# Optimization experiments

Measured on AMD Instinct MI355X. Metric: run time of the kernel, lower is better.

The kernel has to match this reference:

```python
import jax, jax.numpy as jnp
import numpy as np

Q, B, N, DIM, HEADS, CODES = 4, 8, 4096, 1024, 8, 1024
DH = DIM // HEADS  # codebook_dim = 128
SCALE = DH ** -0.5


def setup_inputs() -> dict:
    key = jax.random.key(0)
    k0, k1, k2, k3 = jax.random.split(key, 4)
    return {
        "x": jax.random.normal(k0, (B, N, DIM), jnp.float32),
        "codes": jax.random.normal(k1, (Q, HEADS, CODES, DH), jnp.float32),
        "wk": jax.random.normal(k2, (Q, HEADS, DH, DH), jnp.float32) * SCALE,
        "wv": jax.random.normal(k3, (Q, HEADS, DH, DH), jnp.float32) * SCALE,
    }


def _memcodes_layer(x, codes, wk, wv):
    """One Memcodes quantizer (eval path: hard argmax).
    x: [B,N,DIM]; codes: [H,C,DH]; wk/wv: [H,DH,DH].
    Returns quantized [B,N,DIM], indices [B,H,N]."""
    b, n, _ = x.shape
    q = x.reshape(b, n, HEADS, DH).transpose(0, 2, 1, 3) * SCALE  # [b,h,n,d]
    k = jnp.einsum('hnd,hdc->hnc', codes, wk)  # [h,C,d]
    v = jnp.einsum('hnd,hdc->hnc', codes, wv)  # [h,C,d]
    logits = jnp.einsum('bhid,hjd->bhij', q, k)  # [b,h,n,C]
    idx = jnp.argmax(logits, axis=-1)  # [b,h,n]
    # one_hot(idx) @ v == gather rows of v at idx
    out = jnp.take_along_axis(v[None], idx[..., None], axis=2)  # [b,h,n,d]
    out = out.transpose(0, 2, 1, 3).reshape(b, n, DIM)
    return out, idx


def reference(x, codes, wk, wv):
    residual = x
    quantized_out = jnp.zeros_like(x)
    all_indices = []
    for i in range(Q):  # fixed small loop over quantizer layers
        quantized, idx = _memcodes_layer(residual, codes[i], wk[i], wv[i])
        residual = residual - quantized
        quantized_out = quantized_out + quantized
        all_indices.append(idx)
    return quantized_out, jnp.stack(all_indices, axis=-1)  # [B,N,DIM], [B,H,N,Q]
```

## Files before the change

### kernel.cpp

```cpp
#include <hip/hip_runtime.h>
#include <math.h>

#define QL 4
#define BB 8
#define NN 4096
#define DIMF 1024
#define HH 8
#define CC 1024
#define DH 128

#define MARGIN 4e-3f

typedef __attribute__((ext_vector_type(4))) float f32x4;
typedef __attribute__((ext_vector_type(8))) short s16x8;

__device__ __forceinline__ unsigned short f2bf(float f) {
    unsigned int u = __float_as_uint(f);
    u = u + 0x7fffu + ((u >> 16) & 1u);
    return (unsigned short)(u >> 16);
}
__device__ __forceinline__ float bf2f(unsigned short b) {
    return __uint_as_float(((unsigned int)b) << 16);
}
__device__ __forceinline__ void dma16(const void* g, void* l) {
    __builtin_amdgcn_global_load_lds(
        (const __attribute__((address_space(1))) unsigned int*)g,
        (__attribute__((address_space(3))) unsigned int*)l, 16, 0, 0);
}

#define MFMA(a, bb, c) c = __builtin_amdgcn_mfma_f32_16x16x32_bf16(a, bb, c, 0, 0, 0)

__device__ __forceinline__ void upd(float& m1, float& m2, int& mi, float v, int c) {
    m2 = fmaxf(fminf(m1, v), m2);
    if (v > m1) { m1 = v; mi = c; }
}

__global__ __launch_bounds__(128) void kv_kernel(
    const float* __restrict__ codes, const float* __restrict__ wk,
    const float* __restrict__ wv, unsigned short* __restrict__ khi,
    unsigned short* __restrict__ klo, float* __restrict__ vbuf)
{
    __shared__ float sc[8][128];
    int bid = blockIdx.x;
    int cg  = bid & 127;
    int qh  = bid >> 7;
    int t   = threadIdx.x;

    const float* cbase = codes + ((size_t)qh * CC + (size_t)cg * 8) * DH;
    #pragma unroll
    for (int i = 0; i < 8; ++i) sc[i][t] = cbase[i * DH + t];
    __syncthreads();

    const float* wkb = wk + (size_t)qh * DH * DH;
    const float* wvb = wv + (size_t)qh * DH * DH;

    float ak[8], av[8];
    #pragma unroll
    for (int i = 0; i < 8; ++i) { ak[i] = 0.f; av[i] = 0.f; }

    for (int d = 0; d < DH; ++d) {
        float a = wkb[d * DH + t];
        float b = wvb[d * DH + t];
        #pragma unroll
        for (int i = 0; i < 8; ++i) {
            ak[i] = fmaf(sc[i][d], a, ak[i]);
            av[i] = fmaf(sc[i][d], b, av[i]);
        }
    }

    size_t base = ((size_t)qh * CC + (size_t)cg * 8) * DH + t;
    #pragma unroll
    for (int i = 0; i < 8; ++i) {
        float f = ak[i];
        unsigned short hb = f2bf(f);
        unsigned short lb = f2bf(f - bf2f(hb));
        khi[base + (size_t)i * DH]  = hb;
        klo[base + (size_t)i * DH]  = lb;
        vbuf[base + (size_t)i * DH] = av[i];
    }
}

__global__ __launch_bounds__(256, 2) void fused_kernel(
    const float* __restrict__ x, const unsigned short* __restrict__ khi,
    const unsigned short* __restrict__ klo, const float* __restrict__ vbuf,
    const float* __restrict__ codes, const float* __restrict__ wk,
    const float* __restrict__ wv, float* __restrict__ out)
{
    __shared__ __align__(16) char kstage[2][16384];
    __shared__ int    chosen[64];
    __shared__ float  smax1[64];
    __shared__ int    flagged[64];
    __shared__ int    hist[QL][64];
    __shared__ int    nflag;
    __shared__ float  rbuf32[DH];
    __shared__ double rbuf64[DH];
    __shared__ double pbuf[DH];
    __shared__ int    cand[64];
    __shared__ int    ncand;
    __shared__ int    bestc;
    __shared__ double bestv;

    const int t  = threadIdx.x;
    const int w  = t >> 6;
    const int l  = t & 63;
    const int lr = l & 15;
    const int lg = l >> 4;

    const int bid = blockIdx.x;
    const int h   = bid & 7;
    const int nt  = (bid >> 3) & 63;
    const int b   = bid >> 9;
    const int n0  = nt * 64;

    const int colE  = ((l & 15) << 4) ^ ((l >> 4) << 4) ^ (((l >> 3) & 1) << 5);
    const int loffE = ((l >> 4) << 8) + colE;
    const int loffO = loffE ^ 0x40;

    s16x8 rhi[4], rlo[4];
    {
        const int tok = w * 16 + lr;
        const float* xp = x + ((size_t)(b * NN + n0 + tok)) * DIMF + h * DH;
        #pragma unroll
        for (int ks = 0; ks < 4; ++ks) {
            const float* p = xp + ks * 32 + lg * 8;
            float4 a = *reinterpret_cast<const float4*>(p);
            float4 c = *reinterpret_cast<const float4*>(p + 4);
            float vv[8] = {a.x, a.y, a.z, a.w, c.x, c.y, c.z, c.w};
            s16x8 hi8, lo8;
            #pragma unroll
            for (int j = 0; j < 8; ++j) {
                unsigned short hb = f2bf(vv[j]);
                unsigned short lb = f2bf(vv[j] - bf2f(hb));
                hi8[j] = (short)hb; lo8[j] = (short)lb;
            }
            rhi[ks] = hi8; rlo[ks] = lo8;
        }
    }
    if (t == 0) nflag = 0;
    __syncthreads();

    for (int q = 0; q < QL; ++q) {
        const unsigned short* khq = khi + (size_t)(q * HH + h) * CC * DH;
        const unsigned short* klq = klo + (size_t)(q * HH + h) * CC * DH;
        const float* vq = vbuf + (size_t)(q * HH + h) * CC * DH;
        const char* khc = (const char*)khq;
        const char* klc = (const char*)klq;

        auto stage4 = [&](int buf, int chunk) {
            const char* gh = khc + chunk * 8192 + w * 2048;
            const char* gl = klc + chunk * 8192 + w * 2048;
            char* lb = &kstage[buf][0] + w * 2048;
            dma16(gh + loffE, lb);
            dma16(gh + 1024 + loffO, lb + 1024);
            dma16(gl + loffE, lb + 8192);
            dma16(gl + 1024 + loffO, lb + 8192 + 1024);
        };

        float bv[4], b2[4];
        int   bi[4];
        #pragma unroll
        for (int r = 0; r < 4; ++r) {
            bv[r] = -INFINITY; b2[r] = -INFINITY; bi[r] = 0;
        }

        stage4(0, 0);

        for (int ct = 0; ct < 32; ++ct) {
            const int cur = ct & 1;
            if (ct < 31) {
                stage4(cur ^ 1, ct + 1);
                asm volatile("s_waitcnt vmcnt(4)" ::: "memory");
            } else {
                asm volatile("s_waitcnt vmcnt(0)" ::: "memory");
            }
            __builtin_amdgcn_sched_barrier(0);
            __builtin_amdgcn_s_barrier();
            __builtin_amdgcn_sched_barrier(0);

            const char* Bb = &kstage[cur][0];
            f32x4 a00 = {0.f,0.f,0.f,0.f}, a01 = {0.f,0.f,0.f,0.f};

            #pragma unroll
            for (int ks = 0; ks < 4; ++ks) {
                const int swz = ((ks * 64 + lg * 16) ^ ((lr & 7) << 4)) ^ ((ks >> 1) << 5);
                const char* p0 = Bb + (lr)      * 256 + swz;
                const char* p1 = Bb + (16 + lr) * 256 + swz;
                s16x8 bh0 = *reinterpret_cast<const s16x8*>(p0);
                s16x8 bh1 = *reinterpret_cast<const s16x8*>(p1);
                s16x8 bl0 = *reinterpret_cast<const s16x8*>(p0 + 8192);
                s16x8 bl1 = *reinterpret_cast<const s16x8*>(p1 + 8192);

                __builtin_amdgcn_s_setprio(1);
                MFMA(rhi[ks], bh0, a00); MFMA(rhi[ks], bh1, a01);
                MFMA(rlo[ks], bh0, a00); MFMA(rlo[ks], bh1, a01);
                MFMA(rhi[ks], bl0, a00); MFMA(rhi[ks], bl1, a01);
                __builtin_amdgcn_s_setprio(0);
            }

            {
                const int cb = ct * 32 + lr;
                #pragma unroll
                for (int r = 0; r < 4; ++r) {
                    upd(bv[r], b2[r], bi[r], a00[r], cb);
                    upd(bv[r], b2[r], bi[r], a01[r], cb + 16);
                }
            }

            __builtin_amdgcn_sched_barrier(0);
            __builtin_amdgcn_s_barrier();
            __builtin_amdgcn_sched_barrier(0);
        }

        #pragma unroll
        for (int r = 0; r < 4; ++r) {
            float m = bv[r]; float m2 = b2[r]; int mi = bi[r];
            #pragma unroll
            for (int off = 1; off <= 8; off <<= 1) {
                float ov = __shfl_xor(m, off);
                int   oi = __shfl_xor(mi, off);
                float o2 = __shfl_xor(m2, off);
                float nm2 = fmaxf(fmaxf(m2, o2), fminf(m, ov));
                if (ov > m || (ov == m && oi < mi)) { m = ov; mi = oi; }
                m2 = nm2;
            }
            if (lr == 0) {
                int tok = w * 16 + lg * 4 + r;
                chosen[tok] = mi; smax1[tok] = m;
                int fl = (m - m2 < MARGIN) ? 1 : 0;
                flagged[tok] = fl;
                if (fl) atomicAdd(&nflag, 1);
            }
        }
        __syncthreads();

        int nf = nflag;
        if (nf) {
            for (int tok = 0; tok < 64; ++tok) {
                if (!flagged[tok]) continue;
                if (t == 0) { ncand = 0; bestc = 0x7fffffff; bestv = -1e300; }
                if (t < DH) {
                    double r = (double)x[((size_t)(b * NN + n0 + tok)) * DIMF + h * DH + t];
                    for (int qq = 0; qq < q; ++qq) {
                        int c = hist[qq][tok];
                        const float* crow = codes + ((size_t)(qq * HH + h) * CC + c) * DH;
                        const float* wcol = wv + (size_t)(qq * HH + h) * DH * DH + t;
                        double acc = 0.0;
                        for (int dd = 0; dd < DH; ++dd)
                            acc += (double)crow[dd] * (double)wcol[(size_t)dd * DH];
                        r -= acc;
                    }
                    rbuf64[t] = r;
                    rbuf32[t] = (float)r;
                }
                __syncthreads();
                float thr = smax1[tok] - MARGIN;
                #pragma unroll
                for (int cc4 = 0; cc4 < 4; ++cc4) {
                    int c = t * 4 + cc4;
                    const unsigned short* kh = khq + (size_t)c * DH;
                    const unsigned short* kl = klq + (size_t)c * DH;
                    float acc = 0.f;
                    for (int d = 0; d < DH; ++d)
                        acc = fmaf(bf2f(kh[d]) + bf2f(kl[d]), rbuf32[d], acc);
                    if (acc >= thr) {
                        int p = atomicAdd(&ncand, 1);
                        if (p < 64) cand[p] = c;
                    }
                }
                __syncthreads();
                int nc = ncand; if (nc > 64) nc = 64;
                for (int ci = 0; ci < nc; ++ci) {
                    int c = cand[ci];
                    if (t < DH) {
                        const float* crow = codes + ((size_t)(q * HH + h) * CC + c) * DH;
                        const float* wcol = wk + (size_t)(q * HH + h) * DH * DH + t;
                        double acc = 0.0;
                        for (int dd = 0; dd < DH; ++dd)
                            acc += (double)crow[dd] * (double)wcol[(size_t)dd * DH];
                        pbuf[t] = acc * rbuf64[t];
                    }
                    __syncthreads();
                    if (t == 0) {
                        double sm = 0.0;
                        for (int dd = 0; dd < DH; ++dd) sm += pbuf[dd];
                        if (sm > bestv || (sm == bestv && c < bestc)) { bestv = sm; bestc = c; }
                    }
                    __syncthreads();
                }
                if (t == 0) chosen[tok] = bestc;
                __syncthreads();
            }
        }

        if (t < 64) hist[q][t] = chosen[t];
        if (t == 0) nflag = 0;

        {
            const int tok = w * 16 + lr;
            const float* vrow = vq + (size_t)chosen[tok] * DH;
            #pragma unroll
            for (int ks = 0; ks < 4; ++ks) {
                const float* p = vrow + ks * 32 + lg * 8;
                float4 a = *reinterpret_cast<const float4*>(p);
                float4 c = *reinterpret_cast<const float4*>(p + 4);
                float vv[8] = {a.x, a.y, a.z, a.w, c.x, c.y, c.z, c.w};
                s16x8 hi8 = rhi[ks], lo8 = rlo[ks], nh, nl;
                #pragma unroll
                for (int j = 0; j < 8; ++j) {
                    float f = bf2f((unsigned short)hi8[j]) +
                              bf2f((unsigned short)lo8[j]) - vv[j];
                    unsigned short hb = f2bf(f);
                    nh[j] = (short)hb;
                    nl[j] = (short)f2bf(f - bf2f(hb));
                }
                rhi[ks] = nh; rlo[ks] = nl;
            }
        }
        __syncthreads();
    }

    {
        const int tok = w * 16 + lr;
        const float* xp = x + ((size_t)(b * NN + n0 + tok)) * DIMF + h * DH;
        float* op = out + ((size_t)(b * NN + n0 + tok)) * DIMF + h * DH;
        #pragma unroll
        for (int ks = 0; ks < 4; ++ks) {
            const float* p = xp + ks * 32 + lg * 8;
            float4 a = *reinterpret_cast<const float4*>(p);
            float4 c = *reinterpret_cast<const float4*>(p + 4);
            s16x8 hi8 = rhi[ks], lo8 = rlo[ks];
            float4 o0, o1;
            o0.x = a.x - (bf2f((unsigned short)hi8[0]) + bf2f((unsigned short)lo8[0]));
            o0.y = a.y - (bf2f((unsigned short)hi8[1]) + bf2f((unsigned short)lo8[1]));
            o0.z = a.z - (bf2f((unsigned short)hi8[2]) + bf2f((unsigned short)lo8[2]));
            o0.w = a.w - (bf2f((unsigned short)hi8[3]) + bf2f((unsigned short)lo8[3]));
            o1.x = c.x - (bf2f((unsigned short)hi8[4]) + bf2f((unsigned short)lo8[4]));
            o1.y = c.y - (bf2f((unsigned short)hi8[5]) + bf2f((unsigned short)lo8[5]));
            o1.z = c.z - (bf2f((unsigned short)hi8[6]) + bf2f((unsigned short)lo8[6]));
            o1.w = c.w - (bf2f((unsigned short)hi8[7]) + bf2f((unsigned short)lo8[7]));
            *reinterpret_cast<float4*>(op + ks * 32 + lg * 8)     = o0;
            *reinterpret_cast<float4*>(op + ks * 32 + lg * 8 + 4) = o1;
        }
    }

    __syncthreads();
    if (t < 64) {
        float4 iv;
        iv.x = (float)hist[0][t];
        iv.y = (float)hist[1][t];
        iv.z = (float)hist[2][t];
        iv.w = (float)hist[3][t];
        float* ip = out + (size_t)BB * NN * DIMF +
                    (((size_t)(b * HH + h) * NN) + n0 + t) * QL;
        *reinterpret_cast<float4*>(ip) = iv;
    }
}

extern "C" void kernel_launch(void* const* d_in, const int* in_sizes, int n_in,
                              void* d_out, int out_size, void* d_ws, size_t ws_size,
                              hipStream_t stream) {
    const float* x     = (const float*)d_in[0];
    const float* codes = (const float*)d_in[1];
    const float* wk    = (const float*)d_in[2];
    const float* wv    = (const float*)d_in[3];
    float* out  = (float*)d_out;

    float* vbuf = (float*)d_ws;
    unsigned short* khi = (unsigned short*)(vbuf + (size_t)QL * HH * CC * DH);
    unsigned short* klo = khi + (size_t)QL * HH * CC * DH;

    kv_kernel<<<QL * HH * CC / 8, 128, 0, stream>>>(codes, wk, wv, khi, klo, vbuf);
    fused_kernel<<<BB * HH * (NN / 64), 256, 0, stream>>>(x, khi, klo, vbuf,
                                                          codes, wk, wv, out);
}
```

Before: 1.069 ms.

## Use triple-buffered 16-code K chunks and drop trailing barrier per tile

The K staging changes from double-buffered 32-code chunks to triple-buffered 16-code chunks, so each iteration loads half as much and the loop runs 64 times. With three buffers, the second barrier at the end of each iteration is removed, because the buffer being refilled is never the one being read. This cuts LDS use and synchronisation per iteration. In exchange there are twice as many iterations, each with fewer MFMAs and a single accumulator chain, which leaves less independent work to hide latency.

```diff
diff --git a/kernel.cpp b/kernel.cpp
--- a/kernel.cpp
+++ b/kernel.cpp
@@ -86,7 +86,7 @@
     const float* __restrict__ codes, const float* __restrict__ wk,
     const float* __restrict__ wv, float* __restrict__ out)
 {
-    __shared__ __align__(16) char kstage[2][16384];
+    __shared__ __align__(16) char kstage[3][8192];
     __shared__ int    chosen[64];
     __shared__ float  smax1[64];
     __shared__ int    flagged[64];
@@ -114,7 +114,7 @@
 
     const int colE  = ((l & 15) << 4) ^ ((l >> 4) << 4) ^ (((l >> 3) & 1) << 5);
     const int loffE = ((l >> 4) << 8) + colE;
-    const int loffO = loffE ^ 0x40;
+    const int loffW = (w & 1) ? (loffE ^ 0x40) : loffE;
 
     s16x8 rhi[4], rlo[4];
     {
@@ -146,14 +146,12 @@
         const char* khc = (const char*)khq;
         const char* klc = (const char*)klq;
 
-        auto stage4 = [&](int buf, int chunk) {
-            const char* gh = khc + chunk * 8192 + w * 2048;
-            const char* gl = klc + chunk * 8192 + w * 2048;
-            char* lb = &kstage[buf][0] + w * 2048;
-            dma16(gh + loffE, lb);
-            dma16(gh + 1024 + loffO, lb + 1024);
-            dma16(gl + loffE, lb + 8192);
-            dma16(gl + 1024 + loffO, lb + 8192 + 1024);
+        auto stage2 = [&](int buf, int chunk) {
+            const char* gh = khc + chunk * 4096 + w * 1024;
+            const char* gl = klc + chunk * 4096 + w * 1024;
+            char* lb = &kstage[buf][0] + w * 1024;
+            dma16(gh + loffW, lb);
+            dma16(gl + loffW, lb + 4096);
         };
 
         float bv[4], b2[4];
@@ -163,13 +161,13 @@
             bv[r] = -INFINITY; b2[r] = -INFINITY; bi[r] = 0;
         }
 
-        stage4(0, 0);
-
-        for (int ct = 0; ct < 32; ++ct) {
-            const int cur = ct & 1;
-            if (ct < 31) {
-                stage4(cur ^ 1, ct + 1);
-                asm volatile("s_waitcnt vmcnt(4)" ::: "memory");
+        stage2(0, 0);
+
+        for (int ct = 0; ct < 64; ++ct) {
+            const int cur = ct % 3;
+            if (ct < 63) {
+                stage2((ct + 1) % 3, ct + 1);
+                asm volatile("s_waitcnt vmcnt(2)" ::: "memory");
             } else {
                 asm volatile("s_waitcnt vmcnt(0)" ::: "memory");
             }
@@ -178,37 +176,28 @@
             __builtin_amdgcn_sched_barrier(0);
 
             const char* Bb = &kstage[cur][0];
-            f32x4 a00 = {0.f,0.f,0.f,0.f}, a01 = {0.f,0.f,0.f,0.f};
+            f32x4 a00 = {0.f,0.f,0.f,0.f};
 
             #pragma unroll
             for (int ks = 0; ks < 4; ++ks) {
                 const int swz = ((ks * 64 + lg * 16) ^ ((lr & 7) << 4)) ^ ((ks >> 1) << 5);
-                const char* p0 = Bb + (lr)      * 256 + swz;
-                const char* p1 = Bb + (16 + lr) * 256 + swz;
+                const char* p0 = Bb + lr * 256 + swz;
                 s16x8 bh0 = *reinterpret_cast<const s16x8*>(p0);
-                s16x8 bh1 = *reinterpret_cast<const s16x8*>(p1);
-                s16x8 bl0 = *reinterpret_cast<const s16x8*>(p0 + 8192);
-                s16x8 bl1 = *reinterpret_cast<const s16x8*>(p1 + 8192);
+                s16x8 bl0 = *reinterpret_cast<const s16x8*>(p0 + 4096);
 
                 __builtin_amdgcn_s_setprio(1);
-                MFMA(rhi[ks], bh0, a00); MFMA(rhi[ks], bh1, a01);
-                MFMA(rlo[ks], bh0, a00); MFMA(rlo[ks], bh1, a01);
-                MFMA(rhi[ks], bl0, a00); MFMA(rhi[ks], bl1, a01);
+                MFMA(rhi[ks], bh0, a00);
+                MFMA(rlo[ks], bh0, a00);
+                MFMA(rhi[ks], bl0, a00);
                 __builtin_amdgcn_s_setprio(0);
             }
 
             {
-                const int cb = ct * 32 + lr;
+                const int cb = ct * 16 + lr;
                 #pragma unroll
-                for (int r = 0; r < 4; ++r) {
+                for (int r = 0; r < 4; ++r)
                     upd(bv[r], b2[r], bi[r], a00[r], cb);
-                    upd(bv[r], b2[r], bi[r], a01[r], cb + 16);
-                }
-            }
-
-            __builtin_amdgcn_sched_barrier(0);
-            __builtin_amdgcn_s_barrier();
-            __builtin_amdgcn_sched_barrier(0);
+            }
         }
 
         #pragma unroll
```

After: 1.176 ms. 10.0% more time.
